# Kernel optimization log

Hardware: AMD Instinct MI355X
Metric: run time of the kernel (lower is better)

Reference implementation:

```python
import jax, jax.numpy as jnp
import numpy as np


def _laplacian_kernel(x, z, bandwidth):
    x_sq = jnp.sum(x * x, axis=-1, keepdims=True)          # [N, 1]
    z_sq = jnp.sum(z * z, axis=-1)[None, :]                # [1, M]
    d2 = x_sq + z_sq - 2.0 * jnp.einsum('nd,md->nm', x, z)  # [N, M]
    d = jnp.sqrt(jnp.maximum(d2, 0.0))
    return jnp.exp(-d / bandwidth)


def setup_inputs() -> dict:
    key = jax.random.key(0)
    k1, k2, k3 = jax.random.split(key, 3)
    N, M, D, Y = 8192, 20000, 1024, 256
    batch = jax.random.normal(k1, (N, D), dtype=jnp.float32)
    centers = jax.random.normal(k2, (M, D), dtype=jnp.float32)
    weight = jax.random.normal(k3, (M, Y), dtype=jnp.float32) * 0.02
    return {"batch": batch, "centers": centers, "weight": weight, "bandwidth": 10}


def reference(batch, centers, weight, bandwidth):
    kmat = _laplacian_kernel(batch, centers, float(bandwidth))  # [N, M]
    pred = kmat @ weight                                        # [N, Y]
    return pred
```

## Files before the change

### kernel.cpp

```cpp
#include <hip/hip_runtime.h>
#include <stdint.h>

#define N_ROWS 8192
#define D_DIM  1024
#define M_CENT 20000
#define M_PAD  20224
#define M_TILES 79
#define Y_DIM  256
#define BM 64
#define BN 256
#define MSPLIT 8
#define TILES_PER_SPLIT 10
#define NKT 32
#define GKT 8
#define NG  4
#define PANEL_X (NKT * 512)
#define NKT_M 632
#define PANEL_W (NKT_M * 512)


typedef __attribute__((ext_vector_type(4))) float  f32x4;
typedef __attribute__((ext_vector_type(8))) __bf16 bf16x8;

__device__ __forceinline__ unsigned short f2bf(float f) {
    union { float f; unsigned u; } v; v.f = f;
    unsigned u = v.u;
    u += 0x7FFFu + ((u >> 16) & 1u);
    return (unsigned short)(u >> 16);
}

__device__ __forceinline__ void gll16(void* lds, const void* g) {
    __builtin_amdgcn_global_load_lds(
        (const __attribute__((address_space(1))) void*)g,
        (__attribute__((address_space(3))) void*)lds, 16, 0, 0);
}

__global__ void pack_rows_kernel(const float* __restrict__ src,
                                 unsigned short* __restrict__ dst,
                                 float* __restrict__ sq, int nrows_valid) {
    int row = blockIdx.x;
    int t = threadIdx.x;
    int p = row >> 4, m = row & 15;
    float s = 0.f;
    ushort4 o = make_ushort4(0, 0, 0, 0);
    if (row < nrows_valid) {
        float4 v = ((const float4*)(src + (size_t)row * D_DIM))[t];
        s = v.x * v.x + v.y * v.y + v.z * v.z + v.w * v.w;
        o.x = f2bf(v.x); o.y = f2bf(v.y); o.z = f2bf(v.z); o.w = f2bf(v.w);
    }
    size_t obase = (size_t)p * PANEL_X + (size_t)(t >> 3) * 512
                 + (size_t)((t >> 1) & 3) * 128 + m * 8 + (t & 1) * 4;
    *(ushort4*)(dst + obase) = o;
    __shared__ float red[4];
    for (int off = 32; off; off >>= 1) s += __shfl_down(s, off, 64);
    if ((t & 63) == 0) red[t >> 6] = s;
    __syncthreads();
    if (t == 0) sq[row] = red[0] + red[1] + red[2] + red[3];
}

__global__ void pack_wT_kernel(const float* __restrict__ w,
                               unsigned short* __restrict__ wTp) {
    __shared__ float tile[32][33];
    int m0 = blockIdx.x * 32;
    int y0 = blockIdx.y * 32;
    int tx = threadIdx.x & 31;
    int ty = threadIdx.x >> 5;
    #pragma unroll
    for (int i = 0; i < 4; ++i) {
        int mm = m0 + ty + i * 8;
        float v = (mm < M_CENT) ? w[(size_t)mm * Y_DIM + y0 + tx] : 0.f;
        tile[tx][ty + i * 8] = v;
    }
    __syncthreads();
    #pragma unroll
    for (int i = 0; i < 4; ++i) {
        int yl = ty + i * 8;
        int p = (y0 >> 4) + (yl >> 4);
        size_t off = (size_t)p * PANEL_W + (size_t)(m0 >> 5) * 512
                   + (size_t)(tx >> 3) * 128 + (yl & 15) * 8 + (tx & 7);
        wTp[off] = f2bf(tile[yl][tx]);
    }
}

__global__ void __launch_bounds__(256, 2)
fused_kernel(const unsigned short* __restrict__ Xp,
             const unsigned short* __restrict__ Zp,
             const unsigned short* __restrict__ WTp,
             const float* __restrict__ xsq,
             const float* __restrict__ zsq,
             const int* __restrict__ bwp,
             float* __restrict__ out) {
    __shared__ unsigned short x_stage[BM * 256];
    __shared__ unsigned short lds_p[BM * BN];

    const int t    = threadIdx.x;
    const int wave = t >> 6;
    const int lane = t & 63;
    const int quad = lane >> 4;
    const int l16  = lane & 15;
    const int lane8 = lane * 8;

    const int row0 = blockIdx.x * BM;
    int mt = blockIdx.y * TILES_PER_SPLIT;
    int mt_end = mt + TILES_PER_SPLIT;
    if (mt_end > M_TILES) mt_end = M_TILES;

    int bwi = *bwp;
    float bw;
    if (bwi > 0 && bwi < 1000000) bw = (float)bwi;
    else { union { int i; float f; } u; u.i = bwi; bw = u.f; }
    const float inv_bw = 1.0f / bw;

    float xsqv[16];
    #pragma unroll
    for (int i = 0; i < 16; ++i)
        xsqv[i] = xsq[row0 + (i >> 2) * 16 + quad * 4 + (i & 3)];

    const int s_it  = t >> 6;
    const int s_l16 = (t & 63) >> 2;
    const int s_quad = t & 3;
    const unsigned short* xsrc = Xp + (size_t)((row0 >> 4) + s_it) * PANEL_X
                               + s_quad * 128 + s_l16 * 8;

    const f32x4 vzero = {0.f, 0.f, 0.f, 0.f};
    f32x4 Oacc[16];
    #pragma unroll
    for (int i = 0; i < 16; ++i) Oacc[i] = vzero;

    #pragma unroll 1
    for (; mt < mt_end; ++mt) {
        const unsigned short* zp0 = Zp + (size_t)(mt * 16 + wave * 4) * PANEL_X + lane8;

        float zqv[4];
        #pragma unroll
        for (int jt = 0; jt < 4; ++jt)
            zqv[jt] = zsq[mt * BN + wave * 64 + jt * 16 + l16];

        f32x4 S[16];
        #pragma unroll
        for (int i = 0; i < 16; ++i) S[i] = vzero;

        bf16x8 ae[4], ao[4], be[4], bo[4];
        #pragma unroll
        for (int j = 0; j < 4; ++j)
            be[j] = *(const bf16x8*)(zp0 + (size_t)j * PANEL_X);

        #pragma unroll 1
        for (int g = 0; g < NG; ++g) {
            __syncthreads();
            const unsigned short* xg = xsrc + (size_t)(g * GKT) * 512;
            #pragma unroll
            for (int i = 0; i < GKT; ++i)
                gll16(&x_stage[(i * 256 + t) * 8], xg + (size_t)i * 512);
            __syncthreads();
            #pragma unroll
            for (int i = 0; i < 4; ++i)
                ae[i] = *(const bf16x8*)&x_stage[i * 512 + l16 * 32 + quad * 8];

            #pragma unroll
            for (int kp = 0; kp < GKT / 2; ++kp) {
                const int kt = g * GKT + kp * 2;
                #pragma unroll
                for (int i = 0; i < 4; ++i)
                    ao[i] = *(const bf16x8*)&x_stage[(kp * 2 + 1) * 2048
                                                     + i * 512 + l16 * 32 + quad * 8];
                {
                    const unsigned short* zk = zp0 + (size_t)(kt + 1) * 512;
                    #pragma unroll
                    for (int j = 0; j < 4; ++j)
                        bo[j] = *(const bf16x8*)(zk + (size_t)j * PANEL_X);
                }
                #pragma unroll
                for (int it = 0; it < 4; ++it)
                    #pragma unroll
                    for (int jt = 0; jt < 4; ++jt)
                        S[it * 4 + jt] = __builtin_amdgcn_mfma_f32_16x16x32_bf16(
                            ae[it], be[jt], S[it * 4 + jt], 0, 0, 0);
                if (kp < GKT / 2 - 1) {
                    #pragma unroll
                    for (int i = 0; i < 4; ++i)
                        ae[i] = *(const bf16x8*)&x_stage[(kp * 2 + 2) * 2048
                                                         + i * 512 + l16 * 32 + quad * 8];
                }
                {
                    const unsigned short* zk = zp0 + (size_t)(kt + 2) * 512;
                    #pragma unroll
                    for (int j = 0; j < 4; ++j)
                        be[j] = *(const bf16x8*)(zk + (size_t)j * PANEL_X);
                }
                #pragma unroll
                for (int it = 0; it < 4; ++it)
                    #pragma unroll
                    for (int jt = 0; jt < 4; ++jt)
                        S[it * 4 + jt] = __builtin_amdgcn_mfma_f32_16x16x32_bf16(
                            ao[it], bo[jt], S[it * 4 + jt], 0, 0, 0);
            }
        }

        #pragma unroll
        for (int it = 0; it < 4; ++it) {
            #pragma unroll
            for (int jt = 0; jt < 4; ++jt) {
                f32x4 s4 = S[it * 4 + jt];
                const int col = wave * 64 + jt * 16 + l16;
                const int ch0 = col >> 3, cl = col & 7;
                const float zq = zqv[jt];
                #pragma unroll
                for (int r = 0; r < 4; ++r) {
                    const int row = it * 16 + quad * 4 + r;
                    float d2 = xsqv[it * 4 + r] + zq - 2.0f * s4[r];
                    d2 = fmaxf(d2, 0.f);
                    float p = __expf(-sqrtf(d2) * inv_bw);
                    lds_p[row * 256 + ((ch0 ^ (row & 7)) << 3) + cl] = f2bf(p);
                }
            }
        }
        __syncthreads();

        #pragma unroll
        for (int ks = 0; ks < 8; ++ks) {
            bf16x8 a[4], b[4];
            #pragma unroll
            for (int rt = 0; rt < 4; ++rt) {
                const int row = rt * 16 + l16;
                a[rt] = *(const bf16x8*)&lds_p[row * 256
                          + (((ks * 4 + quad) ^ (l16 & 7)) << 3)];
            }
            #pragma unroll
            for (int ct = 0; ct < 4; ++ct)
                b[ct] = *(const bf16x8*)(WTp + (size_t)(wave * 4 + ct) * PANEL_W
                                             + (size_t)(mt * 8 + ks) * 512 + lane8);
            #pragma unroll
            for (int rt = 0; rt < 4; ++rt)
                #pragma unroll
                for (int ct = 0; ct < 4; ++ct)
                    Oacc[rt * 4 + ct] = __builtin_amdgcn_mfma_f32_16x16x32_bf16(
                        a[rt], b[ct], Oacc[rt * 4 + ct], 0, 0, 0);
        }
    }

    #pragma unroll
    for (int rt = 0; rt < 4; ++rt) {
        #pragma unroll
        for (int ct = 0; ct < 4; ++ct) {
            f32x4 v = Oacc[rt * 4 + ct];
            const int y = wave * 64 + ct * 16 + l16;
            #pragma unroll
            for (int r = 0; r < 4; ++r) {
                const int row = row0 + rt * 16 + quad * 4 + r;
                atomicAdd(&out[(size_t)row * Y_DIM + y], v[r]);
            }
        }
    }
}

extern "C" void kernel_launch(void* const* d_in, const int* in_sizes, int n_in,
                              void* d_out, int out_size, void* d_ws, size_t ws_size,
                              hipStream_t stream) {
    const float* X = (const float*)d_in[0];
    const float* Z = (const float*)d_in[1];
    const float* W = (const float*)d_in[2];
    const int*  bw = (const int*)d_in[3];
    float* out = (float*)d_out;

    char* ws = (char*)d_ws;
    size_t off = 0;
    unsigned short* Xp  = (unsigned short*)(ws + off); off += (size_t)N_ROWS * D_DIM * 2;
    unsigned short* Zp  = (unsigned short*)(ws + off); off += (size_t)M_PAD * D_DIM * 2;
    unsigned short* WTp = (unsigned short*)(ws + off); off += (size_t)Y_DIM * M_PAD * 2;
    float* xsq = (float*)(ws + off); off += (size_t)N_ROWS * 4;
    float* zsq = (float*)(ws + off); off += (size_t)M_PAD * 4;

    hipMemsetAsync(d_out, 0, (size_t)out_size * sizeof(float), stream);
    pack_rows_kernel<<<N_ROWS, 256, 0, stream>>>(X, Xp, xsq, N_ROWS);
    pack_rows_kernel<<<M_PAD, 256, 0, stream>>>(Z, Zp, zsq, M_CENT);
    pack_wT_kernel<<<dim3(M_PAD / 32, Y_DIM / 32), 256, 0, stream>>>(W, WTp);
    fused_kernel<<<dim3(N_ROWS / BM, MSPLIT), 256, 0, stream>>>(Xp, Zp, WTp, xsq, zsq, bw, out);
}
```

Before: 848.6 us.

## Double-buffer X staging in LDS and grid-stride the packing kernels

The fused kernel now splits the K loop into 8 groups of 4 k-tiles and double-buffers X tiles in LDS. The next group's global-to-LDS load is issued before computing on the current one, which removes the second barrier per group and hides the X load latency. The B operand registers are also rotated in a ping-pong pattern. Separately, the pack kernels switch to a fixed 2048-block grid-stride loop to cut block launch overhead. The LDS footprint stays the same, but the prefetch into buffer 0 across m-tiles relies on barrier ordering, which is a correctness risk.

```diff
diff --git a/kernel.cpp b/kernel.cpp
--- a/kernel.cpp
+++ b/kernel.cpp
@@ -12,8 +12,8 @@
 #define MSPLIT 8
 #define TILES_PER_SPLIT 10
 #define NKT 32
-#define GKT 8
-#define NG  4
+#define GKT 4
+#define NG  8
 #define PANEL_X (NKT * 512)
 #define NKT_M 632
 #define PANEL_W (NKT_M * 512)
@@ -37,48 +37,55 @@
 
 __global__ void pack_rows_kernel(const float* __restrict__ src,
                                  unsigned short* __restrict__ dst,
-                                 float* __restrict__ sq, int nrows_valid) {
-    int row = blockIdx.x;
+                                 float* __restrict__ sq,
+                                 int nrows_valid, int nrows_total) {
+    __shared__ float red[4];
     int t = threadIdx.x;
-    int p = row >> 4, m = row & 15;
-    float s = 0.f;
-    ushort4 o = make_ushort4(0, 0, 0, 0);
-    if (row < nrows_valid) {
-        float4 v = ((const float4*)(src + (size_t)row * D_DIM))[t];
-        s = v.x * v.x + v.y * v.y + v.z * v.z + v.w * v.w;
-        o.x = f2bf(v.x); o.y = f2bf(v.y); o.z = f2bf(v.z); o.w = f2bf(v.w);
-    }
-    size_t obase = (size_t)p * PANEL_X + (size_t)(t >> 3) * 512
-                 + (size_t)((t >> 1) & 3) * 128 + m * 8 + (t & 1) * 4;
-    *(ushort4*)(dst + obase) = o;
-    __shared__ float red[4];
-    for (int off = 32; off; off >>= 1) s += __shfl_down(s, off, 64);
-    if ((t & 63) == 0) red[t >> 6] = s;
-    __syncthreads();
-    if (t == 0) sq[row] = red[0] + red[1] + red[2] + red[3];
+    for (int row = blockIdx.x; row < nrows_total; row += gridDim.x) {
+        int p = row >> 4, m = row & 15;
+        float s = 0.f;
+        ushort4 o = make_ushort4(0, 0, 0, 0);
+        if (row < nrows_valid) {
+            float4 v = ((const float4*)(src + (size_t)row * D_DIM))[t];
+            s = v.x * v.x + v.y * v.y + v.z * v.z + v.w * v.w;
+            o.x = f2bf(v.x); o.y = f2bf(v.y); o.z = f2bf(v.z); o.w = f2bf(v.w);
+        }
+        size_t obase = (size_t)p * PANEL_X + (size_t)(t >> 3) * 512
+                     + (size_t)((t >> 1) & 3) * 128 + m * 8 + (t & 1) * 4;
+        *(ushort4*)(dst + obase) = o;
+        for (int off = 32; off; off >>= 1) s += __shfl_down(s, off, 64);
+        if ((t & 63) == 0) red[t >> 6] = s;
+        __syncthreads();
+        if (t == 0) sq[row] = red[0] + red[1] + red[2] + red[3];
+        __syncthreads();
+    }
 }
 
 __global__ void pack_wT_kernel(const float* __restrict__ w,
                                unsigned short* __restrict__ wTp) {
     __shared__ float tile[32][33];
-    int m0 = blockIdx.x * 32;
-    int y0 = blockIdx.y * 32;
     int tx = threadIdx.x & 31;
     int ty = threadIdx.x >> 5;
-    #pragma unroll
-    for (int i = 0; i < 4; ++i) {
-        int mm = m0 + ty + i * 8;
-        float v = (mm < M_CENT) ? w[(size_t)mm * Y_DIM + y0 + tx] : 0.f;
-        tile[tx][ty + i * 8] = v;
-    }
-    __syncthreads();
-    #pragma unroll
-    for (int i = 0; i < 4; ++i) {
-        int yl = ty + i * 8;
-        int p = (y0 >> 4) + (yl >> 4);
-        size_t off = (size_t)p * PANEL_W + (size_t)(m0 >> 5) * 512
-                   + (size_t)(tx >> 3) * 128 + (yl & 15) * 8 + (tx & 7);
-        wTp[off] = f2bf(tile[yl][tx]);
+    const int nblk = (M_PAD / 32) * (Y_DIM / 32);
+    for (int bid = blockIdx.x; bid < nblk; bid += gridDim.x) {
+        int m0 = (bid % (M_PAD / 32)) * 32;
+        int y0 = (bid / (M_PAD / 32)) * 32;
+        #pragma unroll
+        for (int i = 0; i < 4; ++i) {
+            int mm = m0 + ty + i * 8;
+            float v = (mm < M_CENT) ? w[(size_t)mm * Y_DIM + y0 + tx] : 0.f;
+            tile[tx][ty + i * 8] = v;
+        }
+        __syncthreads();
+        #pragma unroll
+        for (int i = 0; i < 4; ++i) {
+            int yl = ty + i * 8;
+            int p = (y0 >> 4) + (yl >> 4);
+            size_t off = (size_t)p * PANEL_W + (size_t)(m0 >> 5) * 512
+                       + (size_t)(tx >> 3) * 128 + (yl & 15) * 8 + (tx & 7);
+            wTp[off] = f2bf(tile[yl][tx]);
+        }
+        __syncthreads();
     }
 }
 
@@ -90,7 +97,7 @@
              const float* __restrict__ zsq,
              const int* __restrict__ bwp,
              float* __restrict__ out) {
-    __shared__ unsigned short x_stage[BM * 256];
+    __shared__ unsigned short x_stage[2][GKT * 4 * 512];
     __shared__ unsigned short lds_p[BM * BN];
 
     const int t    = threadIdx.x;
@@ -117,15 +124,17 @@
         xsqv[i] = xsq[row0 + (i >> 2) * 16 + quad * 4 + (i & 3)];
 
     const int s_it  = t >> 6;
-    const int s_l16 = (t & 63) >> 2;
-    const int s_quad = t & 3;
     const unsigned short* xsrc = Xp + (size_t)((row0 >> 4) + s_it) * PANEL_X
-                               + s_quad * 128 + s_l16 * 8;
+                               + (t & 3) * 128 + ((t & 63) >> 2) * 8;
 
     const f32x4 vzero = {0.f, 0.f, 0.f, 0.f};
     f32x4 Oacc[16];
     #pragma unroll
     for (int i = 0; i < 16; ++i) Oacc[i] = vzero;
+
+    #pragma unroll
+    for (int i = 0; i < GKT; ++i)
+        gll16(&x_stage[0][(i * 256 + t) * 8], xsrc + (size_t)i * 512);
 
     #pragma unroll 1
     for (; mt < mt_end; ++mt) {
@@ -140,60 +149,61 @@
         #pragma unroll
         for (int i = 0; i < 16; ++i) S[i] = vzero;
 
-        bf16x8 ae[4], ao[4], be[4], bo[4];
-        #pragma unroll
-        for (int j = 0; j < 4; ++j)
-            be[j] = *(const bf16x8*)(zp0 + (size_t)j * PANEL_X);
+        bf16x8 bA[4], bB[4];
+        #pragma unroll
+        for (int j = 0; j < 4; ++j) {
+            bA[j] = *(const bf16x8*)(zp0 + (size_t)j * PANEL_X);
+            bB[j] = *(const bf16x8*)(zp0 + 512 + (size_t)j * PANEL_X);
+        }
 
         #pragma unroll 1
         for (int g = 0; g < NG; ++g) {
             __syncthreads();
-            const unsigned short* xg = xsrc + (size_t)(g * GKT) * 512;
-            #pragma unroll
-            for (int i = 0; i < GKT; ++i)
-                gll16(&x_stage[(i * 256 + t) * 8], xg + (size_t)i * 512);
-            __syncthreads();
+            if (g < NG - 1) {
+                const unsigned short* xg = xsrc + (size_t)((g + 1) * GKT) * 512;
+                const int nb = (g + 1) & 1;
+                #pragma unroll
+                for (int i = 0; i < GKT; ++i)
+                    gll16(&x_stage[nb][(i * 256 + t) * 8], xg + (size_t)i * 512);
+            } else if (mt + 1 < mt_end) {
+                #pragma unroll
+                for (int i = 0; i < GKT; ++i)
+                    gll16(&x_stage[0][(i * 256 + t) * 8], xsrc + (size_t)i * 512);
+            }
+
+            const unsigned short* xs = &x_stage[g & 1][0];
+            bf16x8 a0[4], a1[4];
             #pragma unroll
             for (int i = 0; i < 4; ++i)
-                ae[i] = *(const bf16x8*)&x_stage[i * 512 + l16 * 32 + quad * 8];
-
-            #pragma unroll
-            for (int kp = 0; kp < GKT / 2; ++kp) {
-                const int kt = g * GKT + kp * 2;
-                #pragma unroll
-                for (int i = 0; i < 4; ++i)
-                    ao[i] = *(const bf16x8*)&x_stage[(kp * 2 + 1) * 2048
-                                                     + i * 512 + l16 * 32 + quad * 8];
-                {
-                    const unsigned short* zk = zp0 + (size_t)(kt + 1) * 512;
+                a0[i] = *(const bf16x8*)&xs[i * 512 + l16 * 32 + quad * 8];
+
+            #pragma unroll
+            for (int ktl = 0; ktl < GKT; ++ktl) {
+                const int kt = g * GKT + ktl;
+                if (ktl < GKT - 1) {
                     #pragma unroll
-                    for (int j = 0; j < 4; ++j)
-                        bo[j] = *(const bf16x8*)(zk + (size_t)j * PANEL_X);
+                    for (int i = 0; i < 4; ++i) {
+                        bf16x8 v = *(const bf16x8*)&xs[((ktl + 1) * 4 + i) * 512
+                                                       + l16 * 32 + quad * 8];
+                        if (ktl & 1) a0[i] = v; else a1[i] = v;
+                    }
                 }
                 #pragma unroll
                 for (int it = 0; it < 4; ++it)
                     #pragma unroll
                     for (int jt = 0; jt < 4; ++jt)
                         S[it * 4 + jt] = __builtin_amdgcn_mfma_f32_16x16x32_bf16(
-                            ae[it], be[jt], S[it * 4 + jt], 0, 0, 0);
-                if (kp < GKT / 2 - 1) {
-                    #pragma unroll
-                    for (int i = 0; i < 4; ++i)
-                        ae[i] = *(const bf16x8*)&x_stage[(kp * 2 + 2) * 2048
-                                                         + i * 512 + l16 * 32 + quad * 8];
-                }
+                            (ktl & 1) ? a1[it] : a0[it],
+                            (ktl & 1) ? bB[jt] : bA[jt],
+                            S[it * 4 + jt], 0, 0, 0);
                 {
                     const unsigned short* zk = zp0 + (size_t)(kt + 2) * 512;
                     #pragma unroll
-                    for (int j = 0; j < 4; ++j)
-                        be[j] = *(const bf16x8*)(zk + (size_t)j * PANEL_X);
+                    for (int j = 0; j < 4; ++j) {
+                        bf16x8 v = *(const bf16x8*)(zk + (size_t)j * PANEL_X);
+                        if (ktl & 1) bB[j] = v; else bA[j] = v;
+                    }
                 }
-                #pragma unroll
-                for (int it = 0; it < 4; ++it)
-                    #pragma unroll
-                    for (int jt = 0; jt < 4; ++jt)
-                        S[it * 4 + jt] = __builtin_amdgcn_mfma_f32_16x16x32_bf16(
-                            ao[it], bo[jt], S[it * 4 + jt], 0, 0, 0);
             }
         }
 
@@ -272,8 +282,8 @@
     float* zsq = (float*)(ws + off); off += (size_t)M_PAD * 4;
 
     hipMemsetAsync(d_out, 0, (size_t)out_size * sizeof(float), stream);
-    pack_rows_kernel<<<N_ROWS, 256, 0, stream>>>(X, Xp, xsq, N_ROWS);
-    pack_rows_kernel<<<M_PAD, 256, 0, stream>>>(Z, Zp, zsq, M_CENT);
-    pack_wT_kernel<<<dim3(M_PAD / 32, Y_DIM / 32), 256, 0, stream>>>(W, WTp);
+    pack_rows_kernel<<<2048, 256, 0, stream>>>(X, Xp, xsq, N_ROWS, N_ROWS);
+    pack_rows_kernel<<<2048, 256, 0, stream>>>(Z, Zp, zsq, M_CENT, M_PAD);
+    pack_wT_kernel<<<2048, 256, 0, stream>>>(W, WTp);
     fused_kernel<<<dim3(N_ROWS / BM, MSPLIT), 256, 0, stream>>>(Xp, Zp, WTp, xsq, zsq, bw, out);
 }
```

New measurement: 886.6 us. +4.5%, slower.
